# Kernel optimization log

Hardware: AMD Instinct MI355X
Metric: run time of the kernel (lower is better)

The kernel has to match this reference:

```python
import jax, jax.numpy as jnp
import numpy as np

B, S, D, H = 2, 2048, 1024, 16
DK = D // H


def setup_inputs() -> dict:
    key = jax.random.key(0)
    ks = jax.random.split(key, 11)
    sc = 0.02
    return {
        "q": jax.random.normal(ks[0], (B, S, D), jnp.float32),
        "k": jax.random.normal(ks[1], (B, S, D), jnp.float32),
        "v": jax.random.normal(ks[2], (B, S, D), jnp.float32),
        "mask": jnp.ones((1, 1, S, S), jnp.int32),
        "w_q": jax.random.normal(ks[3], (D, D), jnp.float32) * sc,
        "b_q": jnp.zeros((D,), jnp.float32),
        "w_k": jax.random.normal(ks[4], (D, D), jnp.float32) * sc,
        "b_k": jnp.zeros((D,), jnp.float32),
        "w_v": jax.random.normal(ks[5], (D, D), jnp.float32) * sc,
        "b_v": jnp.zeros((D,), jnp.float32),
        "w_o": jax.random.normal(ks[6], (D, D), jnp.float32) * sc,
        "b_o": jnp.zeros((D,), jnp.float32),
    }


def reference(q, k, v, mask, w_q, b_q, w_k, b_k, w_v, b_v, w_o, b_o):
    # projections (torch Linear: x @ W.T + b)
    Q = q @ w_q.T + b_q
    K = k @ w_k.T + b_k
    V = v @ w_v.T + b_v
    # [B,S,D] -> [B,H,S,DK]
    Q = Q.reshape(B, S, H, DK).transpose(0, 2, 1, 3)
    K = K.reshape(B, S, H, DK).transpose(0, 2, 1, 3)
    V = V.reshape(B, S, H, DK).transpose(0, 2, 1, 3)
    scores = jnp.einsum('bhqd,bhkd->bhqk', Q, K) / jnp.sqrt(jnp.float32(DK))
    scores = jnp.where(mask == 0, jnp.float32(-1e9), scores)
    attn = jax.nn.softmax(scores, axis=-1)  # dropout p=0.0 -> identity
    X = jnp.einsum('bhqk,bhkd->bhqd', attn, V)
    X = X.transpose(0, 2, 1, 3).reshape(B, S, D)
    return X @ w_o.T + b_o
```

## Files before the change

### kernel.cpp

```cpp
#include <hip/hip_runtime.h>
#include <cstdint>
#include <cstddef>


typedef __attribute__((ext_vector_type(8))) short short8;
typedef __attribute__((ext_vector_type(4))) float float4v;
typedef __attribute__((ext_vector_type(4))) unsigned short us4;

#define DEV __device__ __forceinline__
#define MFMA16(a, b, c) __builtin_amdgcn_mfma_f32_16x16x32_bf16((a), (b), (c), 0, 0, 0)

DEV unsigned short f2bf(float f) {
  union { float f; unsigned u; } c; c.f = f;
  unsigned u = c.u + 0x7fffu + ((c.u >> 16) & 1u);
  return (unsigned short)(u >> 16);
}

DEV void async16(const void* g, void* l) {
  __builtin_amdgcn_global_load_lds(
      (__attribute__((address_space(1))) void*)(uintptr_t)g,
      (__attribute__((address_space(3))) void*)l, 16, 0, 0);
}

struct CvtJob { const float* src; unsigned short* dst; int n; };
struct CvtArgs { CvtJob job[7]; };

__global__ __launch_bounds__(256) void cvt_bf16_kernel(CvtArgs args) {
  CvtJob j = args.job[blockIdx.y];
  int i = (blockIdx.x * 256 + threadIdx.x) * 8;
  if (i >= j.n) return;
  float4v a = *(const float4v*)(j.src + i);
  float4v b = *(const float4v*)(j.src + i + 4);
  short8 o;
#pragma unroll
  for (int t = 0; t < 4; ++t) { o[t] = (short)f2bf(a[t]); o[t + 4] = (short)f2bf(b[t]); }
  *(short8*)(j.dst + i) = o;
}

__global__ __launch_bounds__(256) void mask_bits_kernel(const int* __restrict__ mask,
                                                        unsigned long long* __restrict__ bits) {
  int t = blockIdx.x * 256 + threadIdx.x;
  unsigned long long b = __ballot(mask[t] != 0);
  if ((t & 63) == 0) bits[t >> 6] = b;
}

__global__ __launch_bounds__(128) void mask_flags_kernel(const unsigned long long* __restrict__ mb,
                                                         unsigned int* __restrict__ flags) {
  int qb = blockIdx.x >> 5, kt = blockIdx.x & 31;
  int t = threadIdx.x;
  unsigned long long w = mb[(size_t)(qb * 128 + t) * 32 + kt];
  unsigned long long b = __ballot(w == ~0ULL);
  __shared__ unsigned int sh[2];
  if ((t & 63) == 0) sh[t >> 6] = (b == ~0ULL) ? 1u : 0u;
  __syncthreads();
  if (t == 0) flags[blockIdx.x] = sh[0] & sh[1];
}

struct GemmJob {
  const unsigned short* A; const unsigned short* W; const float* bias;
  void* out; float scale; int mode;
};
struct GemmArgs { GemmJob job[3]; };

__global__ __launch_bounds__(256, 2) void gemm128_kernel(GemmArgs args) {
  const GemmJob jb = args.job[blockIdx.z];
  const int tid = threadIdx.x;
  const int wave = tid >> 6, lane = tid & 63, lk = lane & 15, quad = lane >> 4;
  const int wm = wave >> 1, wn = wave & 1;
  const int m0 = blockIdx.y * 128, n0 = blockIdx.x * 128;

  __shared__ unsigned short As[128 * 32];
  __shared__ unsigned short Bs[128 * 32];

  float4v acc[4][4] = {};

  const char* Ag = (const char*)jb.A + (size_t)m0 * 2048;
  const char* Wg = (const char*)jb.W + (size_t)n0 * 2048;

#pragma unroll 1
  for (int kk = 0; kk < 32; ++kk) {
    __syncthreads();
    const int kbyte = kk * 64;
#pragma unroll
    for (int i = 0; i < 2; ++i) {
      int o = (wave * 2 + i) * 1024 + lane * 16;
      int r = o >> 6, cb = o & 63;
      async16(Ag + (size_t)r * 2048 + kbyte + cb, (char*)As + (wave * 2 + i) * 1024);
      async16(Wg + (size_t)r * 2048 + kbyte + cb, (char*)Bs + (wave * 2 + i) * 1024);
    }
    __builtin_amdgcn_s_waitcnt(0);
    __syncthreads();

    short8 af[4];
#pragma unroll
    for (int mt = 0; mt < 4; ++mt)
      af[mt] = *(const short8*)(&As[(wm * 64 + mt * 16 + lk) * 32 + quad * 8]);
#pragma unroll
    for (int nt = 0; nt < 4; ++nt) {
      short8 bf = *(const short8*)(&Bs[(wn * 64 + nt * 16 + lk) * 32 + quad * 8]);
#pragma unroll
      for (int mt = 0; mt < 4; ++mt)
        acc[mt][nt] = MFMA16(af[mt], bf, acc[mt][nt]);
    }
  }

  if (jb.mode == 0) {
    unsigned short* outp = (unsigned short*)jb.out;
#pragma unroll
    for (int nt = 0; nt < 4; ++nt) {
      int n = n0 + wn * 64 + nt * 16 + lk;
      float bn = jb.bias[n];
      int h = n >> 6, d = n & 63;
#pragma unroll
      for (int mt = 0; mt < 4; ++mt) {
#pragma unroll
        for (int r = 0; r < 4; ++r) {
          int m = m0 + wm * 64 + mt * 16 + quad * 4 + r;
          int b = m >> 11, s = m & 2047;
          float v = (acc[mt][nt][r] + bn) * jb.scale;
          outp[((size_t)((b * 16 + h) * 2048 + s) << 6) + d] = f2bf(v);
        }
      }
    }
  } else if (jb.mode == 1) {
    float* outp = (float*)jb.out;
#pragma unroll
    for (int nt = 0; nt < 4; ++nt) {
      int n = n0 + wn * 64 + nt * 16 + lk;
      float bn = jb.bias[n];
#pragma unroll
      for (int mt = 0; mt < 4; ++mt) {
#pragma unroll
        for (int r = 0; r < 4; ++r) {
          int m = m0 + wm * 64 + mt * 16 + quad * 4 + r;
          outp[(size_t)m * 1024 + n] = acc[mt][nt][r] + bn;
        }
      }
    }
  } else {
    unsigned short* outp = (unsigned short*)jb.out;
#pragma unroll
    for (int nt = 0; nt < 4; ++nt) {
      int n = n0 + wn * 64 + nt * 16 + lk;
      float bn = jb.bias[n];
      int h = n >> 6, d = n & 63;
#pragma unroll
      for (int mt = 0; mt < 4; ++mt) {
        int m = m0 + wm * 64 + mt * 16 + quad * 4;
        int b = m >> 11, s = m & 2047;
        us4 pk;
#pragma unroll
        for (int r = 0; r < 4; ++r) pk[r] = f2bf(acc[mt][nt][r] + bn);
        *(us4*)(&outp[((size_t)((b * 16 + h) * 64 + d) << 11) + s]) = pk;
      }
    }
  }
}

__global__ __launch_bounds__(256, 2) void attn_kernel(
    const unsigned short* __restrict__ Qp, const unsigned short* __restrict__ Kp,
    const unsigned short* __restrict__ Vtp, const unsigned int* __restrict__ flags,
    const unsigned long long* __restrict__ mbits, unsigned short* __restrict__ Xout) {
  __shared__ unsigned short Qs[128 * 64];
  __shared__ unsigned short Ks[64 * 64];
  __shared__ unsigned short Vts[64 * 64];
  __shared__ unsigned short Ps[128 * 72];
  __shared__ float lsum[128];

  const int tid = threadIdx.x, wave = tid >> 6, lane = tid & 63;
  const int lk = lane & 15, quad = lane >> 4;
  const int bh = blockIdx.y, q0 = blockIdx.x * 128;
  const size_t cbase = (size_t)bh * (2048 * 64);

  {
    const int r8 = lane >> 3, gs = lane & 7;
#pragma unroll
    for (int i = 0; i < 4; ++i) {
      int row = wave * 32 + i * 8 + r8;
      int g = gs ^ (row & 7);
      async16(Qp + cbase + (size_t)(q0 + row) * 64 + g * 8,
              (char*)Qs + (wave * 32 + i * 8) * 128);
    }
  }
  __builtin_amdgcn_s_waitcnt(0);
  __syncthreads();

  short8 qf[2][2];
#pragma unroll
  for (int mt = 0; mt < 2; ++mt)
#pragma unroll
    for (int ks = 0; ks < 2; ++ks) {
      int row = wave * 32 + mt * 16 + lk;
      int gg = (ks * 4 + quad) ^ (lk & 7);
      qf[mt][ks] = *(const short8*)(&Qs[row * 64 + gg * 8]);
    }

  float rs[8];
#pragma unroll
  for (int i = 0; i < 8; ++i) rs[i] = 0.f;
  float4v O[4][2] = {};

#pragma unroll 1
  for (int kt = 0; kt < 32; ++kt) {
    __syncthreads();
    {
      const int r8 = lane >> 3, gs = lane & 7;
#pragma unroll
      for (int i = 0; i < 2; ++i) {
        int row = wave * 16 + i * 8 + r8;
        int g = gs ^ (row & 7);
        async16(Kp + cbase + (size_t)(kt * 64 + row) * 64 + g * 8,
                (char*)Ks + (wave * 16 + i * 8) * 128);
        async16(Vtp + cbase + (size_t)row * 2048 + kt * 64 + g * 8,
                (char*)Vts + (wave * 16 + i * 8) * 128);
      }
    }
    __builtin_amdgcn_s_waitcnt(0);
    __syncthreads();

    float4v sacc[2][4] = {};
#pragma unroll
    for (int nt = 0; nt < 4; ++nt) {
      int krow = nt * 16 + lk;
      short8 kb0 = *(const short8*)(&Ks[krow * 64 + ((quad) ^ (lk & 7)) * 8]);
      short8 kb1 = *(const short8*)(&Ks[krow * 64 + ((4 + quad) ^ (lk & 7)) * 8]);
#pragma unroll
      for (int mt = 0; mt < 2; ++mt) {
        sacc[mt][nt] = MFMA16(qf[mt][0], kb0, sacc[mt][nt]);
        sacc[mt][nt] = MFMA16(qf[mt][1], kb1, sacc[mt][nt]);
      }
    }

    if (__builtin_expect(flags[blockIdx.x * 32 + kt] == 0, 0)) {
#pragma unroll
      for (int i = 0; i < 8; ++i) {
        int row = q0 + wave * 32 + (i >> 2) * 16 + quad * 4 + (i & 3);
        unsigned long long w = mbits[(size_t)row * 32 + kt];
#pragma unroll
        for (int nt = 0; nt < 4; ++nt)
          if (!((w >> (nt * 16 + lk)) & 1ULL))
            sacc[i >> 2][nt][i & 3] = -__builtin_inff();
      }
    }

#pragma unroll
    for (int mt = 0; mt < 2; ++mt)
#pragma unroll
      for (int nt = 0; nt < 4; ++nt)
#pragma unroll
        for (int r = 0; r < 4; ++r) {
          float p = __expf(sacc[mt][nt][r]);
          rs[mt * 4 + r] += p;
          Ps[(wave * 32 + mt * 16 + quad * 4 + r) * 72 + nt * 16 + lk] = f2bf(p);
        }

    short8 pb[2][2];
#pragma unroll
    for (int qt = 0; qt < 2; ++qt)
#pragma unroll
      for (int ks = 0; ks < 2; ++ks)
        pb[qt][ks] = *(const short8*)(&Ps[(wave * 32 + qt * 16 + lk) * 72 + ks * 32 + quad * 8]);
#pragma unroll
    for (int dt = 0; dt < 4; ++dt) {
      int drow = dt * 16 + lk;
      short8 va0 = *(const short8*)(&Vts[drow * 64 + ((quad) ^ (lk & 7)) * 8]);
      short8 va1 = *(const short8*)(&Vts[drow * 64 + ((4 + quad) ^ (lk & 7)) * 8]);
#pragma unroll
      for (int qt = 0; qt < 2; ++qt) {
        O[dt][qt] = MFMA16(va0, pb[qt][0], O[dt][qt]);
        O[dt][qt] = MFMA16(va1, pb[qt][1], O[dt][qt]);
      }
    }
  }

#pragma unroll
  for (int i = 0; i < 8; ++i) {
    float s = rs[i];
    s += __shfl_xor(s, 1); s += __shfl_xor(s, 2);
    s += __shfl_xor(s, 4); s += __shfl_xor(s, 8);
    rs[i] = s;
  }
  if (lk == 0) {
#pragma unroll
    for (int i = 0; i < 8; ++i)
      lsum[wave * 32 + (i >> 2) * 16 + quad * 4 + (i & 3)] = rs[i];
  }
  __syncthreads();
  float linv[2];
#pragma unroll
  for (int qt = 0; qt < 2; ++qt) linv[qt] = 1.f / lsum[wave * 32 + qt * 16 + lk];

  const int b = bh >> 4, h = bh & 15;
#pragma unroll
  for (int dt = 0; dt < 4; ++dt)
#pragma unroll
    for (int qt = 0; qt < 2; ++qt) {
      int s = q0 + wave * 32 + qt * 16 + lk;
      us4 pk;
#pragma unroll
      for (int rr = 0; rr < 4; ++rr) pk[rr] = f2bf(O[dt][qt][rr] * linv[qt]);
      *(us4*)(&Xout[((size_t)(b * 2048 + s)) * 1024 + h * 64 + dt * 16 + quad * 4]) = pk;
    }
}

extern "C" void kernel_launch(void* const* d_in, const int* in_sizes, int n_in,
                              void* d_out, int out_size, void* d_ws, size_t ws_size,
                              hipStream_t stream) {
  const float* q   = (const float*)d_in[0];
  const float* k   = (const float*)d_in[1];
  const float* v   = (const float*)d_in[2];
  const int*   msk = (const int*)d_in[3];
  const float* w_q = (const float*)d_in[4];
  const float* b_q = (const float*)d_in[5];
  const float* w_k = (const float*)d_in[6];
  const float* b_k = (const float*)d_in[7];
  const float* w_v = (const float*)d_in[8];
  const float* b_v = (const float*)d_in[9];
  const float* w_o = (const float*)d_in[10];
  const float* b_o = (const float*)d_in[11];

  char* ws = (char*)d_ws;
  const size_t MB = (size_t)1 << 20;
  unsigned short* q_bf  = (unsigned short*)(ws + 0 * MB);
  unsigned short* k_bf  = (unsigned short*)(ws + 8 * MB);
  unsigned short* v_bf  = (unsigned short*)(ws + 16 * MB);
  unsigned short* wq_bf = (unsigned short*)(ws + 24 * MB);
  unsigned short* wk_bf = (unsigned short*)(ws + 26 * MB);
  unsigned short* wv_bf = (unsigned short*)(ws + 28 * MB);
  unsigned short* wo_bf = (unsigned short*)(ws + 30 * MB);
  unsigned short* Qp    = (unsigned short*)(ws + 32 * MB);
  unsigned short* Kp    = (unsigned short*)(ws + 40 * MB);
  unsigned short* Vtp   = (unsigned short*)(ws + 48 * MB);
  unsigned short* Xa    = (unsigned short*)(ws + 56 * MB);
  unsigned long long* mb = (unsigned long long*)(ws + 64 * MB);
  unsigned int* mflags   = (unsigned int*)(ws + 64 * MB + (512 << 10));

  CvtArgs ca;
  ca.job[0] = { q,   q_bf,  4096 * 1024 };
  ca.job[1] = { k,   k_bf,  4096 * 1024 };
  ca.job[2] = { v,   v_bf,  4096 * 1024 };
  ca.job[3] = { w_q, wq_bf, 1024 * 1024 };
  ca.job[4] = { w_k, wk_bf, 1024 * 1024 };
  ca.job[5] = { w_v, wv_bf, 1024 * 1024 };
  ca.job[6] = { w_o, wo_bf, 1024 * 1024 };
  cvt_bf16_kernel<<<dim3(2048, 7), 256, 0, stream>>>(ca);

  mask_bits_kernel<<<dim3(16384), 256, 0, stream>>>(msk, mb);
  mask_flags_kernel<<<dim3(512), 128, 0, stream>>>(mb, mflags);

  GemmArgs ga;
  ga.job[0] = { q_bf, wq_bf, b_q, (void*)Qp,  0.125f, 0 };
  ga.job[1] = { k_bf, wk_bf, b_k, (void*)Kp,  1.0f,   0 };
  ga.job[2] = { v_bf, wv_bf, b_v, (void*)Vtp, 1.0f,   2 };
  gemm128_kernel<<<dim3(8, 32, 3), 256, 0, stream>>>(ga);

  attn_kernel<<<dim3(16, 32), 256, 0, stream>>>(Qp, Kp, Vtp, mflags, mb, Xa);

  GemmArgs go;
  go.job[0] = { Xa, wo_bf, b_o, d_out, 1.0f, 1 };
  go.job[1] = go.job[0];
  go.job[2] = go.job[0];
  gemm128_kernel<<<dim3(8, 32, 1), 256, 0, stream>>>(go);
}
```

Measured before the change: 263.9 us.

## Double-buffer K/V in attention, fold mask packing into convert, add 64-row output GEMM

The attention loop now double-buffers K and V tiles in LDS, prefetching tile kt+1 while computing tile kt, so global load latency can overlap the MFMA work. Mask bit packing moves into the bf16 convert launch as an extra job, removing one kernel launch. The output projection gets a dedicated 64x128-tile GEMM launched on twice as many blocks to improve occupancy. The softmax also truncates P to bf16 instead of rounding, and accumulates the row sum from the truncated value so it stays consistent with P; the double buffer costs extra LDS.

```diff
diff --git a/kernel.cpp b/kernel.cpp
--- a/kernel.cpp
+++ b/kernel.cpp
@@ -22,26 +22,32 @@
       (__attribute__((address_space(3))) void*)l, 16, 0, 0);
 }
 
-struct CvtJob { const float* src; unsigned short* dst; int n; };
-struct CvtArgs { CvtJob job[7]; };
+struct CvtJob { const float* src; unsigned short* dst; int n; int mode; };
+struct CvtArgs { CvtJob job[8]; };
 
 __global__ __launch_bounds__(256) void cvt_bf16_kernel(CvtArgs args) {
   CvtJob j = args.job[blockIdx.y];
   int i = (blockIdx.x * 256 + threadIdx.x) * 8;
   if (i >= j.n) return;
-  float4v a = *(const float4v*)(j.src + i);
-  float4v b = *(const float4v*)(j.src + i + 4);
-  short8 o;
-#pragma unroll
-  for (int t = 0; t < 4; ++t) { o[t] = (short)f2bf(a[t]); o[t + 4] = (short)f2bf(b[t]); }
-  *(short8*)(j.dst + i) = o;
-}
-
-__global__ __launch_bounds__(256) void mask_bits_kernel(const int* __restrict__ mask,
-                                                        unsigned long long* __restrict__ bits) {
-  int t = blockIdx.x * 256 + threadIdx.x;
-  unsigned long long b = __ballot(mask[t] != 0);
-  if ((t & 63) == 0) bits[t >> 6] = b;
+  if (j.mode == 0) {
+    float4v a = *(const float4v*)(j.src + i);
+    float4v b = *(const float4v*)(j.src + i + 4);
+    short8 o;
+#pragma unroll
+    for (int t = 0; t < 4; ++t) { o[t] = (short)f2bf(a[t]); o[t + 4] = (short)f2bf(b[t]); }
+    *(short8*)(j.dst + i) = o;
+  } else {
+    const int* mi = (const int*)j.src + i;
+    int4 a = ((const int4*)mi)[0], b = ((const int4*)mi)[1];
+    unsigned bits = (a.x != 0 ? 1u : 0) | (a.y != 0 ? 2u : 0) | (a.z != 0 ? 4u : 0) |
+                    (a.w != 0 ? 8u : 0) | (b.x != 0 ? 16u : 0) | (b.y != 0 ? 32u : 0) |
+                    (b.z != 0 ? 64u : 0) | (b.w != 0 ? 128u : 0);
+    unsigned long long w = (unsigned long long)bits << ((threadIdx.x & 7) * 8);
+    w |= __shfl_xor(w, 1);
+    w |= __shfl_xor(w, 2);
+    w |= __shfl_xor(w, 4);
+    if ((threadIdx.x & 7) == 0) ((unsigned long long*)j.dst)[i >> 6] = w;
+  }
 }
 
 __global__ __launch_bounds__(128) void mask_flags_kernel(const unsigned long long* __restrict__ mb,
@@ -122,21 +128,6 @@
         }
       }
     }
-  } else if (jb.mode == 1) {
-    float* outp = (float*)jb.out;
-#pragma unroll
-    for (int nt = 0; nt < 4; ++nt) {
-      int n = n0 + wn * 64 + nt * 16 + lk;
-      float bn = jb.bias[n];
-#pragma unroll
-      for (int mt = 0; mt < 4; ++mt) {
-#pragma unroll
-        for (int r = 0; r < 4; ++r) {
-          int m = m0 + wm * 64 + mt * 16 + quad * 4 + r;
-          outp[(size_t)m * 1024 + n] = acc[mt][nt][r] + bn;
-        }
-      }
-    }
   } else {
     unsigned short* outp = (unsigned short*)jb.out;
 #pragma unroll
@@ -152,6 +143,68 @@
 #pragma unroll
         for (int r = 0; r < 4; ++r) pk[r] = f2bf(acc[mt][nt][r] + bn);
         *(us4*)(&outp[((size_t)((b * 16 + h) * 64 + d) << 11) + s]) = pk;
+      }
+    }
+  }
+}
+
+__global__ __launch_bounds__(256, 2) void gemm_out64_kernel(
+    const unsigned short* __restrict__ A, const unsigned short* __restrict__ W,
+    const float* __restrict__ bias, float* __restrict__ out) {
+  const int tid = threadIdx.x;
+  const int wave = tid >> 6, lane = tid & 63, lk = lane & 15, quad = lane >> 4;
+  const int wm = wave >> 1, wn = wave & 1;
+  const int m0 = blockIdx.y * 64, n0 = blockIdx.x * 128;
+
+  __shared__ unsigned short As[64 * 32];
+  __shared__ unsigned short Bs[128 * 32];
+
+  float4v acc[2][4] = {};
+
+  const char* Ag = (const char*)A + (size_t)m0 * 2048;
+  const char* Wg = (const char*)W + (size_t)n0 * 2048;
+
+#pragma unroll 1
+  for (int kk = 0; kk < 32; ++kk) {
+    __syncthreads();
+    const int kbyte = kk * 64;
+    {
+      int o = wave * 1024 + lane * 16;
+      int r = o >> 6, cb = o & 63;
+      async16(Ag + (size_t)r * 2048 + kbyte + cb, (char*)As + wave * 1024);
+    }
+#pragma unroll
+    for (int i = 0; i < 2; ++i) {
+      int o = (wave * 2 + i) * 1024 + lane * 16;
+      int r = o >> 6, cb = o & 63;
+      async16(Wg + (size_t)r * 2048 + kbyte + cb, (char*)Bs + (wave * 2 + i) * 1024);
+    }
+    __builtin_amdgcn_s_waitcnt(0);
+    __syncthreads();
+
+    short8 af[2];
+#pragma unroll
+    for (int mt = 0; mt < 2; ++mt)
+      af[mt] = *(const short8*)(&As[(wm * 32 + mt * 16 + lk) * 32 + quad * 8]);
+#pragma unroll
+    for (int nt = 0; nt < 4; ++nt) {
+      short8 bf = *(const short8*)(&Bs[(wn * 64 + nt * 16 + lk) * 32 + quad * 8]);
+#pragma unroll
+      for (int mt = 0; mt < 2; ++mt)
+        acc[mt][nt] = MFMA16(af[mt], bf, acc[mt][nt]);
+    }
+  }
+
+#pragma unroll
+  for (int nt = 0; nt < 4; ++nt) {
+    int n = n0 + wn * 64 + nt * 16 + lk;
+    float bn = bias[n];
+#pragma unroll
+    for (int mt = 0; mt < 2; ++mt) {
+#pragma unroll
+      for (int r = 0; r < 4; ++r) {
+        int m = m0 + wm * 32 + mt * 16 + quad * 4 + r;
+        out[(size_t)m * 1024 + n] = acc[mt][nt][r] + bn;
       }
     }
   }
@@ -162,8 +215,8 @@
     const unsigned short* __restrict__ Vtp, const unsigned int* __restrict__ flags,
     const unsigned long long* __restrict__ mbits, unsigned short* __restrict__ Xout) {
   __shared__ unsigned short Qs[128 * 64];
-  __shared__ unsigned short Ks[64 * 64];
-  __shared__ unsigned short Vts[64 * 64];
+  __shared__ unsigned short Ks[2][64 * 64];
+  __shared__ unsigned short Vts[2][64 * 64];
   __shared__ unsigned short Ps[128 * 72];
   __shared__ float lsum[128];
 
@@ -171,16 +224,21 @@
   const int lk = lane & 15, quad = lane >> 4;
   const int bh = blockIdx.y, q0 = blockIdx.x * 128;
   const size_t cbase = (size_t)bh * (2048 * 64);
-
-  {
-    const int r8 = lane >> 3, gs = lane & 7;
-#pragma unroll
-    for (int i = 0; i < 4; ++i) {
-      int row = wave * 32 + i * 8 + r8;
-      int g = gs ^ (row & 7);
-      async16(Qp + cbase + (size_t)(q0 + row) * 64 + g * 8,
-              (char*)Qs + (wave * 32 + i * 8) * 128);
-    }
+  const int r8 = lane >> 3, gs = lane & 7;
+
+#pragma unroll
+  for (int i = 0; i < 4; ++i) {
+    int row = wave * 32 + i * 8 + r8;
+    int g = gs ^ (row & 7);
+    async16(Qp + cbase + (size_t)(q0 + row) * 64 + g * 8,
+            (char*)Qs + (wave * 32 + i * 8) * 128);
+  }
+#pragma unroll
+  for (int i = 0; i < 2; ++i) {
+    int row = wave * 16 + i * 8 + r8;
+    int g = gs ^ (row & 7);
+    async16(Kp + cbase + (size_t)row * 64 + g * 8, (char*)&Ks[0][0] + (wave * 16 + i * 8) * 128);
+    async16(Vtp + cbase + (size_t)row * 2048 + g * 8, (char*)&Vts[0][0] + (wave * 16 + i * 8) * 128);
   }
   __builtin_amdgcn_s_waitcnt(0);
   __syncthreads();
@@ -202,28 +260,25 @@
 
 #pragma unroll 1
   for (int kt = 0; kt < 32; ++kt) {
-    __syncthreads();
-    {
-      const int r8 = lane >> 3, gs = lane & 7;
+    const int cur = kt & 1;
+    if (kt < 31) {
 #pragma unroll
       for (int i = 0; i < 2; ++i) {
         int row = wave * 16 + i * 8 + r8;
         int g = gs ^ (row & 7);
-        async16(Kp + cbase + (size_t)(kt * 64 + row) * 64 + g * 8,
-                (char*)Ks + (wave * 16 + i * 8) * 128);
-        async16(Vtp + cbase + (size_t)row * 2048 + kt * 64 + g * 8,
-                (char*)Vts + (wave * 16 + i * 8) * 128);
-      }
-    }
-    __builtin_amdgcn_s_waitcnt(0);
-    __syncthreads();
+        async16(Kp + cbase + (size_t)((kt + 1) * 64 + row) * 64 + g * 8,
+                (char*)&Ks[cur ^ 1][0] + (wave * 16 + i * 8) * 128);
+        async16(Vtp + cbase + (size_t)row * 2048 + (kt + 1) * 64 + g * 8,
+                (char*)&Vts[cur ^ 1][0] + (wave * 16 + i * 8) * 128);
+      }
+    }
 
     float4v sacc[2][4] = {};
 #pragma unroll
     for (int nt = 0; nt < 4; ++nt) {
       int krow = nt * 16 + lk;
-      short8 kb0 = *(const short8*)(&Ks[krow * 64 + ((quad) ^ (lk & 7)) * 8]);
-      short8 kb1 = *(const short8*)(&Ks[krow * 64 + ((4 + quad) ^ (lk & 7)) * 8]);
+      short8 kb0 = *(const short8*)(&Ks[cur][krow * 64 + ((quad) ^ (lk & 7)) * 8]);
+      short8 kb1 = *(const short8*)(&Ks[cur][krow * 64 + ((4 + quad) ^ (lk & 7)) * 8]);
 #pragma unroll
       for (int mt = 0; mt < 2; ++mt) {
         sacc[mt][nt] = MFMA16(qf[mt][0], kb0, sacc[mt][nt]);
@@ -250,8 +305,10 @@
 #pragma unroll
         for (int r = 0; r < 4; ++r) {
           float p = __expf(sacc[mt][nt][r]);
-          rs[mt * 4 + r] += p;
-          Ps[(wave * 32 + mt * 16 + quad * 4 + r) * 72 + nt * 16 + lk] = f2bf(p);
+          unsigned pu = __float_as_uint(p);
+          rs[mt * 4 + r] += __uint_as_float(pu & 0xffff0000u);
+          Ps[(wave * 32 + mt * 16 + quad * 4 + r) * 72 + nt * 16 + lk] =
+              (unsigned short)(pu >> 16);
         }
 
     short8 pb[2][2];
@@ -263,14 +320,17 @@
 #pragma unroll
     for (int dt = 0; dt < 4; ++dt) {
       int drow = dt * 16 + lk;
-      short8 va0 = *(const short8*)(&Vts[drow * 64 + ((quad) ^ (lk & 7)) * 8]);
-      short8 va1 = *(const short8*)(&Vts[drow * 64 + ((4 + quad) ^ (lk & 7)) * 8]);
+      short8 va0 = *(const short8*)(&Vts[cur][drow * 64 + ((quad) ^ (lk & 7)) * 8]);
+      short8 va1 = *(const short8*)(&Vts[cur][drow * 64 + ((4 + quad) ^ (lk & 7)) * 8]);
 #pragma unroll
       for (int qt = 0; qt < 2; ++qt) {
         O[dt][qt] = MFMA16(va0, pb[qt][0], O[dt][qt]);
         O[dt][qt] = MFMA16(va1, pb[qt][1], O[dt][qt]);
       }
     }
+
+    __builtin_amdgcn_s_waitcnt(0x0f70);
+    __syncthreads();
   }
 
 #pragma unroll
@@ -336,16 +396,16 @@
   unsigned int* mflags   = (unsigned int*)(ws + 64 * MB + (512 << 10));
 
   CvtArgs ca;
-  ca.job[0] = { q,   q_bf,  4096 * 1024 };
-  ca.job[1] = { k,   k_bf,  4096 * 1024 };
-  ca.job[2] = { v,   v_bf,  4096 * 1024 };
-  ca.job[3] = { w_q, wq_bf, 1024 * 1024 };
-  ca.job[4] = { w_k, wk_bf, 1024 * 1024 };
-  ca.job[5] = { w_v, wv_bf, 1024 * 1024 };
-  ca.job[6] = { w_o, wo_bf, 1024 * 1024 };
-  cvt_bf16_kernel<<<dim3(2048, 7), 256, 0, stream>>>(ca);
-
-  mask_bits_kernel<<<dim3(16384), 256, 0, stream>>>(msk, mb);
+  ca.job[0] = { q,   q_bf,  4096 * 1024, 0 };
+  ca.job[1] = { k,   k_bf,  4096 * 1024, 0 };
+  ca.job[2] = { v,   v_bf,  4096 * 1024, 0 };
+  ca.job[3] = { w_q, wq_bf, 1024 * 1024, 0 };
+  ca.job[4] = { w_k, wk_bf, 1024 * 1024, 0 };
+  ca.job[5] = { w_v, wv_bf, 1024 * 1024, 0 };
+  ca.job[6] = { w_o, wo_bf, 1024 * 1024, 0 };
+  ca.job[7] = { (const float*)msk, (unsigned short*)mb, 2048 * 2048, 1 };
+  cvt_bf16_kernel<<<dim3(2048, 8), 256, 0, stream>>>(ca);
+
   mask_flags_kernel<<<dim3(512), 128, 0, stream>>>(mb, mflags);
 
   GemmArgs ga;
@@ -356,9 +416,5 @@
 
   attn_kernel<<<dim3(16, 32), 256, 0, stream>>>(Qp, Kp, Vtp, mflags, mb, Xa);
 
-  GemmArgs go;
-  go.job[0] = { Xa, wo_bf, b_o, d_out, 1.0f, 1 };
-  go.job[1] = go.job[0];
-  go.job[2] = go.job[0];
-  gemm128_kernel<<<dim3(8, 32, 1), 256, 0, stream>>>(go);
-}
+  gemm_out64_kernel<<<dim3(8, 64), 256, 0, stream>>>(Xa, wo_bf, b_o, (float*)d_out);
+}
```

Result: faster. 254.6 us (-3.5%).
